# Performance work log

Hardware: AMD Instinct MI355X
Metric: run time of the kernel (lower is better)

The kernel has to match this reference:

```python
import jax, jax.numpy as jnp
import numpy as np

EMBED_DIM = 1024
NUM_HEADS = 16
HEAD_DIM = EMBED_DIM // NUM_HEADS


def setup_inputs() -> dict:
    key = jax.random.key(0)
    ks = jax.random.split(key, 9)
    B, T, D = 2, 4096, EMBED_DIM
    scale = 1.0 / np.sqrt(D)
    x = jax.random.normal(ks[0], (B, T, D), dtype=jnp.float32)
    # nn.Linear weights stored as (out, in); we use (in, out) layout via transpose-free init
    Wq = jax.random.uniform(ks[1], (D, D), dtype=jnp.float32, minval=-scale, maxval=scale)
    Wk = jax.random.uniform(ks[2], (D, D), dtype=jnp.float32, minval=-scale, maxval=scale)
    Wv = jax.random.uniform(ks[3], (D, D), dtype=jnp.float32, minval=-scale, maxval=scale)
    Wo = jax.random.uniform(ks[4], (D, D), dtype=jnp.float32, minval=-scale, maxval=scale)
    bq = jax.random.uniform(ks[5], (D,), dtype=jnp.float32, minval=-scale, maxval=scale)
    bk = jax.random.uniform(ks[6], (D,), dtype=jnp.float32, minval=-scale, maxval=scale)
    bv = jax.random.uniform(ks[7], (D,), dtype=jnp.float32, minval=-scale, maxval=scale)
    bo = jax.random.uniform(ks[8], (D,), dtype=jnp.float32, minval=-scale, maxval=scale)
    return {"x": x, "Wq": Wq, "bq": bq, "Wk": Wk, "bk": bk,
            "Wv": Wv, "bv": bv, "Wo": Wo, "bo": bo}


def reference(x, Wq, bq, Wk, bk, Wv, bv, Wo, bo):
    B, T, D = x.shape
    H, Hd = NUM_HEADS, HEAD_DIM
    q = x @ Wq + bq  # [B,T,D]
    k = x @ Wk + bk
    v = x @ Wv + bv
    # [B,T,D] -> [B,H,T,Hd]
    q = q.reshape(B, T, H, Hd).transpose(0, 2, 1, 3)
    k = k.reshape(B, T, H, Hd).transpose(0, 2, 1, 3)
    v = v.reshape(B, T, H, Hd).transpose(0, 2, 1, 3)
    att = jnp.einsum('bhqd,bhkd->bhqk', q, k) / jnp.sqrt(jnp.float32(Hd))
    causal = jnp.tril(jnp.ones((T, T), dtype=bool))  # True = keep
    att = jnp.where(causal, att, -jnp.inf)
    att = jax.nn.softmax(att, axis=-1)
    out = jnp.einsum('bhqk,bhkd->bhqd', att, v)  # [B,H,T,Hd]
    out = out.transpose(0, 2, 1, 3).reshape(B, T, D)
    return out @ Wo + bo
```

## Files before the change

### kernel.cpp

```cpp
#include <hip/hip_runtime.h>
#include <hip/hip_bf16.h>
#include <math.h>

typedef __bf16 bf16;
typedef __attribute__((ext_vector_type(8))) __bf16 bf16x8;
typedef __attribute__((ext_vector_type(4))) __bf16 bf16x4;
typedef __attribute__((ext_vector_type(4))) short short4v;
typedef __attribute__((ext_vector_type(4))) float f32x4;

#define MFMA16(a,b,c)  __builtin_amdgcn_mfma_f32_16x16x32_bf16((a),(b),(c),0,0,0)
#define MFMAK16(a,b,c) __builtin_amdgcn_mfma_f32_16x16x16bf16_1k((a),(b),(c),0,0,0)

__device__ __forceinline__ void gload16(const void* gp, void* lp) {
  __builtin_amdgcn_global_load_lds(
      (const __attribute__((address_space(1))) void*)gp,
      (__attribute__((address_space(3))) void*)lp, 16, 0, 0);
}

__global__ __launch_bounds__(256) void cast_x(
    const float* __restrict__ x, bf16* __restrict__ xb)
{
  size_t i = ((size_t)blockIdx.x*256 + threadIdx.x) * 8;
  f32x4 a = *(const f32x4*)(x+i);
  f32x4 b = *(const f32x4*)(x+i+4);
  bf16x8 o;
  #pragma unroll
  for (int j=0;j<4;j++) { o[j] = (bf16)a[j]; o[4+j] = (bf16)b[j]; }
  *(bf16x8*)(xb+i) = o;
}

__global__ __launch_bounds__(1024) void tr_cast(
    const float* __restrict__ w0, const float* __restrict__ w1,
    const float* __restrict__ w2, bf16* __restrict__ dst)
{
  __shared__ bf16 tile[64][65];
  const float* src = (blockIdx.z==0)?w0:(blockIdx.z==1)?w1:w2;
  bf16* d = dst + (size_t)blockIdx.z * (1024*1024);
  int x = threadIdx.x, y = threadIdx.y;
  int tc = blockIdx.x, tr = blockIdx.y;
  #pragma unroll
  for (int i=0;i<4;i++) {
    int r = y + i*16;
    tile[r][x] = (bf16)src[(size_t)(tr*64+r)*1024 + tc*64 + x];
  }
  __syncthreads();
  #pragma unroll
  for (int i=0;i<4;i++) {
    int r = y + i*16;
    d[(size_t)(tc*64+r)*1024 + tr*64 + x] = tile[x][r];
  }
}

__global__ __launch_bounds__(256) void gemm_qkv(
    const bf16* __restrict__ A, const bf16* __restrict__ Bt,
    const float* __restrict__ bq, const float* __restrict__ bk, const float* __restrict__ bv,
    bf16* __restrict__ q, bf16* __restrict__ k, bf16* __restrict__ v,
    int M, int K)
{
  __shared__ __align__(16) bf16 As[128*32];
  __shared__ __align__(16) bf16 Bs[128*32];
  const int tid  = threadIdx.x;
  const int wave = tid >> 6;
  const int lane = tid & 63;
  const int l15  = lane & 15;
  const int quad = lane >> 4;
  const int m0 = blockIdx.y * 128;
  const int n0 = blockIdx.x * 128;
  const int wm = (wave >> 1) * 64;
  const int wn = (wave & 1) * 64;
  const int srow = lane >> 2;
  const int scol = (lane & 3) * 8;

  f32x4 acc[4][4];
  #pragma unroll
  for (int i=0;i<4;i++)
    #pragma unroll
    for (int j=0;j<4;j++)
      acc[i][j] = (f32x4){0.f,0.f,0.f,0.f};

  for (int k0 = 0; k0 < K; k0 += 32) {
    __syncthreads();
    #pragma unroll
    for (int p=0;p<2;p++) {
      int c = p*4 + wave;
      int row = c*16 + srow;
      gload16(A  + (size_t)(m0+row)*K + k0 + scol, As + c*512);
      gload16(Bt + (size_t)(n0+row)*K + k0 + scol, Bs + c*512);
    }
    __syncthreads();
    bf16x8 af[4], bfr[4];
    #pragma unroll
    for (int t=0;t<4;t++) {
      af[t]  = *(const bf16x8*)(As + (wm + t*16 + l15)*32 + quad*8);
      bfr[t] = *(const bf16x8*)(Bs + (wn + t*16 + l15)*32 + quad*8);
    }
    #pragma unroll
    for (int mt=0;mt<4;mt++)
      #pragma unroll
      for (int nt=0;nt<4;nt++)
        acc[mt][nt] = MFMA16(af[mt], bfr[nt], acc[mt][nt]);
  }

  const int mat = n0 >> 10;
  const float* bsel = (mat==0) ? bq : (mat==1) ? bk : bv;
  bf16*       osel  = (mat==0) ? q  : (mat==1) ? k  : v;
  #pragma unroll
  for (int nt=0;nt<4;nt++) {
    int col = n0 + wn + nt*16 + l15;
    int cw  = col & 1023;
    float bvv = bsel[cw];
    #pragma unroll
    for (int mt=0;mt<4;mt++) {
      int row = m0 + wm + mt*16 + quad*4;
      #pragma unroll
      for (int r=0;r<4;r++)
        osel[(size_t)(row + r)*1024 + cw] = (bf16)(acc[mt][nt][r] + bvv);
    }
  }
}

__global__ __launch_bounds__(256) void gemm_out(
    const bf16* __restrict__ A, const bf16* __restrict__ Bt,
    const float* __restrict__ bias, float* __restrict__ C,
    int M, int N, int K)
{
  __shared__ __align__(16) bf16 As[128*32];
  __shared__ __align__(16) bf16 Bs[128*32];
  const int tid  = threadIdx.x;
  const int wave = tid >> 6;
  const int lane = tid & 63;
  const int l15  = lane & 15;
  const int quad = lane >> 4;
  const int m0 = blockIdx.y * 128;
  const int n0 = blockIdx.x * 128;
  const int wm = (wave >> 1) * 64;
  const int wn = (wave & 1) * 64;
  const int srow = lane >> 2;
  const int scol = (lane & 3) * 8;

  f32x4 acc[4][4];
  #pragma unroll
  for (int i=0;i<4;i++)
    #pragma unroll
    for (int j=0;j<4;j++)
      acc[i][j] = (f32x4){0.f,0.f,0.f,0.f};

  for (int k0 = 0; k0 < K; k0 += 32) {
    __syncthreads();
    #pragma unroll
    for (int p=0;p<2;p++) {
      int c = p*4 + wave;
      int row = c*16 + srow;
      gload16(A  + (size_t)(m0+row)*K + k0 + scol, As + c*512);
      gload16(Bt + (size_t)(n0+row)*K + k0 + scol, Bs + c*512);
    }
    __syncthreads();
    bf16x8 af[4], bfr[4];
    #pragma unroll
    for (int t=0;t<4;t++) {
      af[t]  = *(const bf16x8*)(As + (wm + t*16 + l15)*32 + quad*8);
      bfr[t] = *(const bf16x8*)(Bs + (wn + t*16 + l15)*32 + quad*8);
    }
    #pragma unroll
    for (int mt=0;mt<4;mt++)
      #pragma unroll
      for (int nt=0;nt<4;nt++)
        acc[mt][nt] = MFMA16(af[mt], bfr[nt], acc[mt][nt]);
  }

  #pragma unroll
  for (int nt=0;nt<4;nt++) {
    int col = n0 + wn + nt*16 + l15;
    float bvv = bias[col];
    #pragma unroll
    for (int mt=0;mt<4;mt++) {
      int row = m0 + wm + mt*16 + quad*4;
      #pragma unroll
      for (int r=0;r<4;r++)
        C[(size_t)(row + r)*N + col] = acc[mt][nt][r] + bvv;
    }
  }
}

__global__ __launch_bounds__(256, 4) void attn_fwd(
    const bf16* __restrict__ Q, const bf16* __restrict__ Kp,
    const bf16* __restrict__ V, bf16* __restrict__ O)
{
  __shared__ __align__(16) bf16 Ks[2*64*72];
  __shared__ __align__(16) bf16 Vt[2*64*72];

  const int tid  = threadIdx.x;
  const int w    = tid >> 6;
  const int lane = tid & 63;
  const int l15  = lane & 15;
  const int quad = lane >> 4;

  const int bid = blockIdx.x;
  const int qt  = 63 - (bid >> 5);
  const int bh  = bid & 31;
  const int h   = bh & 15;
  const int b   = bh >> 4;

  const size_t headoff = (size_t)h * 64;
  const size_t bbase   = (size_t)b * 4096;

  bf16x8 aq[2];
  {
    int row = qt*64 + w*16 + l15;
    const bf16* qp = Q + (bbase + row)*1024 + headoff + quad*8;
    aq[0] = *(const bf16x8*)(qp);
    aq[1] = *(const bf16x8*)(qp + 32);
  }

  short4v ones_s;
  {
    bf16x4 o1;
    #pragma unroll
    for (int j=0;j<4;j++) o1[j] = (bf16)1.0f;
    ones_s = __builtin_bit_cast(short4v, o1);
  }

  f32x4 acco[4];
  f32x4 accli;
  #pragma unroll
  for (int i=0;i<4;i++) acco[i] = (f32x4){0.f,0.f,0.f,0.f};
  accli = (f32x4){0.f,0.f,0.f,0.f};

  const int kt_row = tid >> 2;
  const int kt_col = (tid & 3) * 16;

  {
    const bf16* kp = Kp + (bbase + kt_row)*1024 + headoff + kt_col;
    bf16x8 k0 = *(const bf16x8*)(kp);
    bf16x8 k1 = *(const bf16x8*)(kp + 8);
    *(bf16x8*)(Ks + kt_row*72 + kt_col)     = k0;
    *(bf16x8*)(Ks + kt_row*72 + kt_col + 8) = k1;
    const bf16* vp = V + (bbase + lane)*1024 + headoff + w*16;
    bf16x8 v0 = *(const bf16x8*)(vp);
    bf16x8 v1 = *(const bf16x8*)(vp + 8);
    #pragma unroll
    for (int j=0;j<8;j++) {
      Vt[(w*16 + j    )*72 + lane] = v0[j];
      Vt[(w*16 + 8 + j)*72 + lane] = v1[j];
    }
  }
  __syncthreads();

  for (int kt = 0; kt <= qt; ++kt) {
    const int p = kt & 1;
    const bool pre = (kt < qt);

    bf16x8 kr0, kr1, vr0, vr1;
    if (pre) {
      const bf16* kp = Kp + (bbase + (size_t)(kt+1)*64 + kt_row)*1024 + headoff + kt_col;
      kr0 = *(const bf16x8*)(kp);
      kr1 = *(const bf16x8*)(kp + 8);
      const bf16* vp = V + (bbase + (size_t)(kt+1)*64 + lane)*1024 + headoff + w*16;
      vr0 = *(const bf16x8*)(vp);
      vr1 = *(const bf16x8*)(vp + 8);
    }

    const bf16* ksb = Ks + p*4608;
    const bf16* vtb = Vt + p*4608;

    f32x4 accs[4];
    #pragma unroll
    for (int i=0;i<4;i++) accs[i] = (f32x4){0.f,0.f,0.f,0.f};
    #pragma unroll
    for (int kk=0;kk<2;kk++) {
      #pragma unroll
      for (int tt=0;tt<4;tt++) {
        bf16x8 ka = *(const bf16x8*)(ksb + (tt*16 + l15)*72 + kk*32 + quad*8);
        accs[tt] = MFMA16(ka, aq[kk], accs[tt]);
      }
    }

    const bool diag = (kt == qt);
    short4v pts[4];
    #pragma unroll
    for (int tt=0;tt<4;tt++) {
      bf16x4 pb;
      #pragma unroll
      for (int r=0;r<4;r++) {
        float tv = fminf(accs[tt][r] * 0.1803368801f, 60.0f);
        float pf = exp2f(tv);
        if (diag && (tt*16 + quad*4 + r > w*16 + l15)) pf = 0.0f;
        pb[r] = (bf16)pf;
      }
      pts[tt] = __builtin_bit_cast(short4v, pb);
    }

    #pragma unroll
    for (int nt=0;nt<4;nt++) {
      #pragma unroll
      for (int tt=0;tt<4;tt++) {
        bf16x4 va = *(const bf16x4*)(vtb + (nt*16 + l15)*72 + tt*16 + quad*4);
        acco[nt] = MFMAK16(__builtin_bit_cast(short4v, va), pts[tt], acco[nt]);
      }
    }
    #pragma unroll
    for (int tt=0;tt<4;tt++)
      accli = MFMAK16(ones_s, pts[tt], accli);

    if (pre) {
      bf16* ksn = Ks + (p^1)*4608;
      bf16* vtn = Vt + (p^1)*4608;
      *(bf16x8*)(ksn + kt_row*72 + kt_col)     = kr0;
      *(bf16x8*)(ksn + kt_row*72 + kt_col + 8) = kr1;
      #pragma unroll
      for (int j=0;j<8;j++) {
        vtn[(w*16 + j    )*72 + lane] = vr0[j];
        vtn[(w*16 + 8 + j)*72 + lane] = vr1[j];
      }
      __syncthreads();
    }
  }

  {
    float inv = 1.0f / accli[0];
    int qrow = qt*64 + w*16 + l15;
    bf16* ob = O + (bbase + qrow)*1024 + headoff;
    #pragma unroll
    for (int nt=0;nt<4;nt++) {
      bf16x4 o;
      #pragma unroll
      for (int r=0;r<4;r++) o[r] = (bf16)(acco[nt][r] * inv);
      *(bf16x4*)(ob + nt*16 + quad*4) = o;
    }
  }
}

extern "C" void kernel_launch(void* const* d_in, const int* in_sizes, int n_in,
                              void* d_out, int out_size, void* d_ws, size_t ws_size,
                              hipStream_t stream) {
  const float* x  = (const float*)d_in[0];
  const float* Wq = (const float*)d_in[1];
  const float* bq = (const float*)d_in[2];
  const float* Wk = (const float*)d_in[3];
  const float* bk = (const float*)d_in[4];
  const float* Wv = (const float*)d_in[5];
  const float* bv = (const float*)d_in[6];
  const float* Wo = (const float*)d_in[7];
  const float* bo = (const float*)d_in[8];
  float* out = (float*)d_out;

  bf16* ws = (bf16*)d_ws;
  bf16* q  = ws;
  bf16* k  = q + (size_t)8192*1024;
  bf16* v  = k + (size_t)8192*1024;
  bf16* xb = v + (size_t)8192*1024;
  bf16* ao = q;
  bf16* WtQKV = (bf16*)d_out;
  bf16* WtO   = xb;

  tr_cast<<<dim3(16,16,3), dim3(64,16), 0, stream>>>(Wq, Wk, Wv, WtQKV);
  cast_x<<<4096, 256, 0, stream>>>(x, xb);
  gemm_qkv<<<dim3(24,64), 256, 0, stream>>>(xb, WtQKV, bq, bk, bv, q, k, v, 8192, 1024);
  tr_cast<<<dim3(16,16,1), dim3(64,16), 0, stream>>>(Wo, Wo, Wo, WtO);
  attn_fwd<<<2048, 256, 0, stream>>>(q, k, v, ao);
  gemm_out<<<dim3(8,64), 256, 0, stream>>>(ao, WtO, bo, out, 8192, 1024, 1024);
}
```

Measured before the change: 356.5 us.

## Process 128-row query tiles per attention block and merge weight transpose launches

The attention kernel now gives each block 128 query rows, with each wave owning two 16-row groups. Every K/V tile loaded into shared memory is reused across twice as many queries, and the grid is halved. Groups and tiles that lie entirely above the causal diagonal are skipped, and block indices are interleaved so query tiles of different lengths are spread across the grid. The Wo transpose is folded into a single four-matrix transpose launch that writes to a separate workspace region, which removes one kernel launch but needs more workspace. In exchange, register pressure rises, which may reduce occupancy under the 256,4 launch bounds.

```diff
diff --git a/kernel.cpp b/kernel.cpp
--- a/kernel.cpp
+++ b/kernel.cpp
@@ -29,13 +29,15 @@
   *(bf16x8*)(xb+i) = o;
 }
 
-__global__ __launch_bounds__(1024) void tr_cast(
+__global__ __launch_bounds__(1024) void tr_cast4(
     const float* __restrict__ w0, const float* __restrict__ w1,
-    const float* __restrict__ w2, bf16* __restrict__ dst)
+    const float* __restrict__ w2, const float* __restrict__ w3,
+    bf16* __restrict__ dqkv, bf16* __restrict__ dO)
 {
   __shared__ bf16 tile[64][65];
-  const float* src = (blockIdx.z==0)?w0:(blockIdx.z==1)?w1:w2;
-  bf16* d = dst + (size_t)blockIdx.z * (1024*1024);
+  const int z = blockIdx.z;
+  const float* src = (z==0)?w0:(z==1)?w1:(z==2)?w2:w3;
+  bf16* d = (z<3) ? (dqkv + (size_t)z*(1024*1024)) : dO;
   int x = threadIdx.x, y = threadIdx.y;
   int tc = blockIdx.x, tr = blockIdx.y;
   #pragma unroll
@@ -196,35 +198,42 @@
   const int quad = lane >> 4;
 
   const int bid = blockIdx.x;
-  const int qt  = 63 - (bid >> 5);
   const int bh  = bid & 31;
+  const int j   = bid >> 5;
+  const int a   = j & 7;
+  const int sel = j >> 3;
+  const int qt  = (sel==0) ? a : (sel==1) ? 15-a : (sel==2) ? 16+a : 31-a;
   const int h   = bh & 15;
   const int b   = bh >> 4;
 
   const size_t headoff = (size_t)h * 64;
   const size_t bbase   = (size_t)b * 4096;
 
-  bf16x8 aq[2];
-  {
-    int row = qt*64 + w*16 + l15;
+  bf16x8 aq[2][2];
+  #pragma unroll
+  for (int g=0; g<2; g++) {
+    int row = qt*128 + w*32 + g*16 + l15;
     const bf16* qp = Q + (bbase + row)*1024 + headoff + quad*8;
-    aq[0] = *(const bf16x8*)(qp);
-    aq[1] = *(const bf16x8*)(qp + 32);
+    aq[g][0] = *(const bf16x8*)(qp);
+    aq[g][1] = *(const bf16x8*)(qp + 32);
   }
 
   short4v ones_s;
   {
     bf16x4 o1;
     #pragma unroll
-    for (int j=0;j<4;j++) o1[j] = (bf16)1.0f;
+    for (int jj=0;jj<4;jj++) o1[jj] = (bf16)1.0f;
     ones_s = __builtin_bit_cast(short4v, o1);
   }
 
-  f32x4 acco[4];
-  f32x4 accli;
-  #pragma unroll
-  for (int i=0;i<4;i++) acco[i] = (f32x4){0.f,0.f,0.f,0.f};
-  accli = (f32x4){0.f,0.f,0.f,0.f};
+  f32x4 acco[2][4];
+  f32x4 accli[2];
+  #pragma unroll
+  for (int g=0; g<2; g++) {
+    accli[g] = (f32x4){0.f,0.f,0.f,0.f};
+    #pragma unroll
+    for (int i=0;i<4;i++) acco[g][i] = (f32x4){0.f,0.f,0.f,0.f};
+  }
 
   const int kt_row = tid >> 2;
   const int kt_col = (tid & 3) * 16;
@@ -239,16 +248,20 @@
     bf16x8 v0 = *(const bf16x8*)(vp);
     bf16x8 v1 = *(const bf16x8*)(vp + 8);
     #pragma unroll
-    for (int j=0;j<8;j++) {
-      Vt[(w*16 + j    )*72 + lane] = v0[j];
-      Vt[(w*16 + 8 + j)*72 + lane] = v1[j];
+    for (int jj=0;jj<8;jj++) {
+      Vt[(w*16 + jj    )*72 + lane] = v0[jj];
+      Vt[(w*16 + 8 + jj)*72 + lane] = v1[jj];
     }
   }
   __syncthreads();
 
-  for (int kt = 0; kt <= qt; ++kt) {
+  const int ktmax = 2*qt + 1;
+  const int qlo0  = qt*128 + w*32;
+  const int qhi_w = qlo0 + 31;
+
+  for (int kt = 0; kt <= ktmax; ++kt) {
     const int p = kt & 1;
-    const bool pre = (kt < qt);
+    const bool pre = (kt < ktmax);
 
     bf16x8 kr0, kr1, vr0, vr1;
     if (pre) {
@@ -260,47 +273,62 @@
       vr1 = *(const bf16x8*)(vp + 8);
     }
 
-    const bf16* ksb = Ks + p*4608;
-    const bf16* vtb = Vt + p*4608;
-
-    f32x4 accs[4];
-    #pragma unroll
-    for (int i=0;i<4;i++) accs[i] = (f32x4){0.f,0.f,0.f,0.f};
-    #pragma unroll
-    for (int kk=0;kk<2;kk++) {
+    const int t0 = kt*64;
+    if (t0 <= qhi_w) {
+      const bf16* ksb = Ks + p*4608;
+      const bf16* vtb = Vt + p*4608;
+
+      short4v pts[2][4];
+      bool alive[2];
+      #pragma unroll
+      for (int g=0; g<2; g++) {
+        const int qlo_g = qlo0 + g*16;
+        alive[g] = (t0 <= qlo_g + 15);
+        if (alive[g]) {
+          f32x4 accs[4];
+          #pragma unroll
+          for (int i=0;i<4;i++) accs[i] = (f32x4){0.f,0.f,0.f,0.f};
+          #pragma unroll
+          for (int kk=0;kk<2;kk++) {
+            #pragma unroll
+            for (int tt=0;tt<4;tt++) {
+              bf16x8 ka = *(const bf16x8*)(ksb + (tt*16 + l15)*72 + kk*32 + quad*8);
+              accs[tt] = MFMA16(ka, aq[g][kk], accs[tt]);
+            }
+          }
+          const bool needs_mask = (t0 + 63 > qlo_g);
+          const int qg = qlo_g + l15;
+          #pragma unroll
+          for (int tt=0;tt<4;tt++) {
+            bf16x4 pb;
+            #pragma unroll
+            for (int r=0;r<4;r++) {
+              float tv = fminf(accs[tt][r] * 0.1803368801f, 60.0f);
+              float pf = exp2f(tv);
+              if (needs_mask && (t0 + tt*16 + quad*4 + r > qg)) pf = 0.0f;
+              pb[r] = (bf16)pf;
+            }
+            pts[g][tt] = __builtin_bit_cast(short4v, pb);
+          }
+        }
+      }
+
+      #pragma unroll
+      for (int nt=0;nt<4;nt++) {
+        #pragma unroll
+        for (int tt=0;tt<4;tt++) {
+          bf16x4 va = *(const bf16x4*)(vtb + (nt*16 + l15)*72 + tt*16 + quad*4);
+          short4v vas = __builtin_bit_cast(short4v, va);
+          acco[0][nt] = MFMAK16(vas, pts[0][tt], acco[0][nt]);
+          if (alive[1]) acco[1][nt] = MFMAK16(vas, pts[1][tt], acco[1][nt]);
+        }
+      }
       #pragma unroll
       for (int tt=0;tt<4;tt++) {
-        bf16x8 ka = *(const bf16x8*)(ksb + (tt*16 + l15)*72 + kk*32 + quad*8);
-        accs[tt] = MFMA16(ka, aq[kk], accs[tt]);
+        accli[0] = MFMAK16(ones_s, pts[0][tt], accli[0]);
+        if (alive[1]) accli[1] = MFMAK16(ones_s, pts[1][tt], accli[1]);
       }
     }
-
-    const bool diag = (kt == qt);
-    short4v pts[4];
-    #pragma unroll
-    for (int tt=0;tt<4;tt++) {
-      bf16x4 pb;
-      #pragma unroll
-      for (int r=0;r<4;r++) {
-        float tv = fminf(accs[tt][r] * 0.1803368801f, 60.0f);
-        float pf = exp2f(tv);
-        if (diag && (tt*16 + quad*4 + r > w*16 + l15)) pf = 0.0f;
-        pb[r] = (bf16)pf;
-      }
-      pts[tt] = __builtin_bit_cast(short4v, pb);
-    }
-
-    #pragma unroll
-    for (int nt=0;nt<4;nt++) {
-      #pragma unroll
-      for (int tt=0;tt<4;tt++) {
-        bf16x4 va = *(const bf16x4*)(vtb + (nt*16 + l15)*72 + tt*16 + quad*4);
-        acco[nt] = MFMAK16(__builtin_bit_cast(short4v, va), pts[tt], acco[nt]);
-      }
-    }
-    #pragma unroll
-    for (int tt=0;tt<4;tt++)
-      accli = MFMAK16(ones_s, pts[tt], accli);
 
     if (pre) {
       bf16* ksn = Ks + (p^1)*4608;
@@ -308,23 +336,24 @@
       *(bf16x8*)(ksn + kt_row*72 + kt_col)     = kr0;
       *(bf16x8*)(ksn + kt_row*72 + kt_col + 8) = kr1;
       #pragma unroll
-      for (int j=0;j<8;j++) {
-        vtn[(w*16 + j    )*72 + lane] = vr0[j];
-        vtn[(w*16 + 8 + j)*72 + lane] = vr1[j];
+      for (int jj=0;jj<8;jj++) {
+        vtn[(w*16 + jj    )*72 + lane] = vr0[jj];
+        vtn[(w*16 + 8 + jj)*72 + lane] = vr1[jj];
       }
       __syncthreads();
     }
   }
 
-  {
-    float inv = 1.0f / accli[0];
-    int qrow = qt*64 + w*16 + l15;
+  #pragma unroll
+  for (int g=0; g<2; g++) {
+    float inv = 1.0f / accli[g][0];
+    int qrow = qt*128 + w*32 + g*16 + l15;
     bf16* ob = O + (bbase + qrow)*1024 + headoff;
     #pragma unroll
     for (int nt=0;nt<4;nt++) {
       bf16x4 o;
       #pragma unroll
-      for (int r=0;r<4;r++) o[r] = (bf16)(acco[nt][r] * inv);
+      for (int r=0;r<4;r++) o[r] = (bf16)(acco[g][nt][r] * inv);
       *(bf16x4*)(ob + nt*16 + quad*4) = o;
     }
   }
@@ -349,14 +378,13 @@
   bf16* k  = q + (size_t)8192*1024;
   bf16* v  = k + (size_t)8192*1024;
   bf16* xb = v + (size_t)8192*1024;
+  bf16* WtO = xb + (size_t)8192*1024;
   bf16* ao = q;
   bf16* WtQKV = (bf16*)d_out;
-  bf16* WtO   = xb;
-
-  tr_cast<<<dim3(16,16,3), dim3(64,16), 0, stream>>>(Wq, Wk, Wv, WtQKV);
+
+  tr_cast4<<<dim3(16,16,4), dim3(64,16), 0, stream>>>(Wq, Wk, Wv, Wo, WtQKV, WtO);
   cast_x<<<4096, 256, 0, stream>>>(x, xb);
   gemm_qkv<<<dim3(24,64), 256, 0, stream>>>(xb, WtQKV, bq, bk, bv, q, k, v, 8192, 1024);
-  tr_cast<<<dim3(16,16,1), dim3(64,16), 0, stream>>>(Wo, Wo, Wo, WtO);
-  attn_fwd<<<2048, 256, 0, stream>>>(q, k, v, ao);
+  attn_fwd<<<1024, 256, 0, stream>>>(q, k, v, ao);
   gemm_out<<<dim3(8,64), 256, 0, stream>>>(ao, WtO, bo, out, 8192, 1024, 1024);
 }
```

Result: slower. 423.2 us (+18.7%).
